# Optimization experiments

Measured on AMD Instinct MI355X. Metric: run time of the kernel, lower is better.

The kernel has to match this reference:

```python
import jax, jax.numpy as jnp
import numpy as np

EPS_LN = 1e-6
NEG_INF = -1e9


def layer_norm(x, gamma, beta, eps=EPS_LN):
    mu = jnp.mean(x, axis=-1, keepdims=True)
    var = jnp.mean(jnp.square(x - mu), axis=-1, keepdims=True)
    return (x - mu) * jax.lax.rsqrt(var + eps) * gamma + beta


def setup_inputs() -> dict:
    key = jax.random.key(0)
    B, S, F, H = 2, 2048, 1024, 16
    D = F // H
    ks = jax.random.split(key, 10)
    s = 1.0 / np.sqrt(F)
    return {
        "x": jax.random.normal(ks[0], (B, S, F), jnp.float32),
        "Wq": jax.random.normal(ks[1], (F, F), jnp.float32) * s,
        "bq": jnp.zeros((F,), jnp.float32),
        "Wk": jax.random.normal(ks[2], (F, F), jnp.float32) * s,
        "bk": jnp.zeros((F,), jnp.float32),
        "Wv": jax.random.normal(ks[3], (F, F), jnp.float32) * s,
        "bv": jnp.zeros((F,), jnp.float32),
        "Wo": jax.random.normal(ks[4], (F, F), jnp.float32) * s,
        "bo": jnp.zeros((F,), jnp.float32),
        "gamma1": jnp.ones((F,), jnp.float32),
        "beta1": jnp.zeros((F,), jnp.float32),
        "gamma2": jnp.ones((F,), jnp.float32),
        "beta2": jnp.zeros((F,), jnp.float32),
        # keras 'uniform' initializer: U(-0.05, 0.05), shape (pos_emb_size=S, depth)
        "pos_emb": jax.random.uniform(ks[5], (S, D), jnp.float32, -0.05, 0.05),
    }


def reference(x, Wq, bq, Wk, bk, Wv, bv, Wo, bo, gamma1, beta1, gamma2, beta2, pos_emb):
    B, S, F = x.shape
    H = 16
    D = F // H
    xn = layer_norm(x, gamma1, beta1)  # pre-LN; also the residual source per original code

    def split_heads(t):
        return t.reshape(B, S, H, D).transpose(0, 2, 1, 3)  # [B,H,S,D]

    q = split_heads(xn @ Wq + bq)
    k = split_heads(xn @ Wk + bk)
    v = split_heads(xn @ Wv + bv)

    # inline position embedding add to K: broadcast [1,1,S,D]
    k = k + pos_emb[None, None, :, :]

    logits = jnp.einsum("bhqd,bhkd->bhqk", q, k) / jnp.sqrt(jnp.float32(D))
    causal = jnp.triu(jnp.ones((S, S), jnp.float32), k=1)  # 1 above diagonal
    logits = logits + causal * NEG_INF
    attn = jax.nn.softmax(logits, axis=-1)  # dropout is identity at inference

    ctx = jnp.einsum("bhqk,bhkd->bhqd", attn, v)
    ctx = ctx.transpose(0, 2, 1, 3).reshape(B, S, F)
    out = ctx @ Wo + bo + xn  # residual with the layernormed input (as in original)
    out = layer_norm(out, gamma2, beta2)
    return out, attn
```

## Files before the change

kernel.cpp:

```cpp
#include <hip/hip_runtime.h>
#include <hip/hip_bf16.h>

#define B_ 2
#define S_ 2048
#define F_ 1024
#define H_ 16
#define D_ 64
#define M_ (B_ * S_)

__global__ void ln_kernel(const float* in, float* out,
                          const float* __restrict__ gamma,
                          const float* __restrict__ beta) {
  int row = blockIdx.x;
  int tid = threadIdx.x;
  const float4* inr = (const float4*)(in + (size_t)row * F_);
  float4 xv = inr[tid];
  float s  = xv.x + xv.y + xv.z + xv.w;
  float s2 = xv.x * xv.x + xv.y * xv.y + xv.z * xv.z + xv.w * xv.w;
#pragma unroll
  for (int off = 32; off > 0; off >>= 1) {
    s  += __shfl_down(s, off, 64);
    s2 += __shfl_down(s2, off, 64);
  }
  __shared__ float red[8];
  int wid = tid >> 6, lane = tid & 63;
  if (lane == 0) { red[wid] = s; red[4 + wid] = s2; }
  __syncthreads();
  if (tid == 0) {
    red[0] = red[0] + red[1] + red[2] + red[3];
    red[4] = red[4] + red[5] + red[6] + red[7];
  }
  __syncthreads();
  float mean = red[0] * (1.0f / F_);
  float var  = red[4] * (1.0f / F_) - mean * mean;
  float rstd = rsqrtf(var + 1e-6f);
  float4 g  = ((const float4*)gamma)[tid];
  float4 be = ((const float4*)beta)[tid];
  float4 o;
  o.x = (xv.x - mean) * rstd * g.x + be.x;
  o.y = (xv.y - mean) * rstd * g.y + be.y;
  o.z = (xv.z - mean) * rstd * g.z + be.z;
  o.w = (xv.w - mean) * rstd * g.w + be.w;
  ((float4*)(out + (size_t)row * F_))[tid] = o;
}

__global__ void gemm_bias(const float* __restrict__ A, const float* __restrict__ W,
                          const float* __restrict__ bias, float* __restrict__ C,
                          const float* R, const float* __restrict__ pos,
                          int mode) {
  const int K = F_, N = F_;
  __shared__ float As[16][132];
  __shared__ float Bs[16][128];
  int tid = threadIdx.x;
  int bm = blockIdx.y * 128, bn = blockIdx.x * 128;
  int tx = tid & 15, ty = tid >> 4;
  float acc[8][8] = {};
  int ar  = tid >> 2;
  int ac  = (tid & 3) << 2;
  int bk  = tid >> 5;
  int bn4 = (tid & 31) << 2;
  const float* Aptr0 = A + (size_t)(bm + ar) * K + ac;
  const float* Aptr1 = Aptr0 + (size_t)64 * K;
  const float* Wptr0 = W + (size_t)bk * N + bn + bn4;
  const float* Wptr1 = Wptr0 + (size_t)8 * N;
  for (int k0 = 0; k0 < K; k0 += 16) {
    float4 a0 = *(const float4*)(Aptr0 + k0);
    float4 a1 = *(const float4*)(Aptr1 + k0);
    float4 b0 = *(const float4*)(Wptr0 + (size_t)k0 * N);
    float4 b1 = *(const float4*)(Wptr1 + (size_t)k0 * N);
    __syncthreads();
    As[ac + 0][ar] = a0.x; As[ac + 1][ar] = a0.y;
    As[ac + 2][ar] = a0.z; As[ac + 3][ar] = a0.w;
    As[ac + 0][ar + 64] = a1.x; As[ac + 1][ar + 64] = a1.y;
    As[ac + 2][ar + 64] = a1.z; As[ac + 3][ar + 64] = a1.w;
    *(float4*)&Bs[bk][bn4]     = b0;
    *(float4*)&Bs[bk + 8][bn4] = b1;
    __syncthreads();
#pragma unroll
    for (int kk = 0; kk < 16; ++kk) {
      float av[8], bv[8];
      *(float4*)(av)     = *(const float4*)&As[kk][ty * 8];
      *(float4*)(av + 4) = *(const float4*)&As[kk][ty * 8 + 4];
      *(float4*)(bv)     = *(const float4*)&Bs[kk][tx * 8];
      *(float4*)(bv + 4) = *(const float4*)&Bs[kk][tx * 8 + 4];
#pragma unroll
      for (int i = 0; i < 8; ++i)
#pragma unroll
        for (int j = 0; j < 8; ++j)
          acc[i][j] += av[i] * bv[j];
    }
  }
#pragma unroll
  for (int i = 0; i < 8; ++i) {
    int m = bm + ty * 8 + i;
#pragma unroll
    for (int j = 0; j < 8; ++j) {
      int n = bn + tx * 8 + j;
      float val = acc[i][j] + bias[n];
      if (mode == 1) val += pos[(size_t)(m & (S_ - 1)) * D_ + (n & (D_ - 1))];
      if (mode == 2) val += R[(size_t)m * N + n];
      C[(size_t)m * N + n] = val;
    }
  }
}

__global__ __launch_bounds__(1024) void attn_kernel(
    const float* q, const float* __restrict__ k, const float* __restrict__ v,
    float* __restrict__ attn, float* ctx, float* __restrict__ rowsum) {
  int bh = blockIdx.y;
  int b = bh >> 4, h = bh & 15;
  int qt = blockIdx.x;
  int tid = threadIdx.x;
  int w = tid >> 6, lane = tid & 63;
  int q_idx = qt * 16 + w;

  __shared__ float K_lds[128][65];
  __shared__ float V_lds[128][64];
  __shared__ float q_lds[16][64];
  __shared__ float p_lds[16][128];

  {
    int r = tid >> 6, c = tid & 63;
    q_lds[r][c] = q[(size_t)(b * S_ + qt * 16 + r) * F_ + h * 64 + c];
  }

  float cacc = 0.0f, ssum = 0.0f;
  int q_max = qt * 16 + 15;
  int nch = (q_max >> 7) + 1;
  const float* Kbase = k + (size_t)b * S_ * F_ + h * 64;
  const float* Vbase = v + (size_t)b * S_ * F_ + h * 64;
  float* arow = attn + ((size_t)bh * S_ + q_idx) * S_;

  for (int c = 0; c < nch; ++c) {
    int base = c << 7;
    __syncthreads();
    for (int idx = tid; idx < 128 * 64; idx += 1024) {
      int r = idx >> 6, cc = idx & 63;
      K_lds[r][cc] = Kbase[(size_t)(base + r) * F_ + cc];
      V_lds[r][cc] = Vbase[(size_t)(base + r) * F_ + cc];
    }
    __syncthreads();
    float acc0 = 0.f, acc1 = 0.f;
#pragma unroll
    for (int d = 0; d < 64; ++d) {
      float qd = q_lds[w][d];
      acc0 += qd * K_lds[lane][d];
      acc1 += qd * K_lds[64 + lane][d];
    }
    int j0 = base + lane, j1 = base + 64 + lane;
    float p0 = 0.f, p1 = 0.f;
    if (j0 <= q_idx) { p0 = __expf(acc0 * 0.125f); arow[j0] = p0; }
    if (j1 <= q_idx) { p1 = __expf(acc1 * 0.125f); arow[j1] = p1; }
    ssum += p0 + p1;
    p_lds[w][lane] = p0;
    p_lds[w][64 + lane] = p1;
    int jmax = q_idx - base + 1;
    if (jmax > 128) jmax = 128;
#pragma unroll 4
    for (int jj = 0; jj < jmax; ++jj)
      cacc += p_lds[w][jj] * V_lds[jj][lane];
  }
  float tot = ssum;
#pragma unroll
  for (int off = 32; off > 0; off >>= 1) tot += __shfl_xor(tot, off, 64);
  float inv = 1.0f / tot;
  ctx[(size_t)(b * S_ + q_idx) * F_ + h * 64 + lane] = cacc * inv;
  if (lane == 0) rowsum[(size_t)bh * S_ + q_idx] = tot;
}

__global__ void rescale_kernel(float* __restrict__ attn,
                               const float* __restrict__ rowsum) {
  int q_idx = blockIdx.x;
  int bh = blockIdx.y;
  float inv = 1.0f / rowsum[(size_t)bh * S_ + q_idx];
  float* arow = attn + ((size_t)bh * S_ + q_idx) * S_;
  int tid = threadIdx.x;
#pragma unroll
  for (int it = 0; it < 2; ++it) {
    int v4 = tid + it * 256;
    int j0 = v4 << 2;
    float4 val;
    if (j0 + 3 <= q_idx) {
      val = ((const float4*)arow)[v4];
      val.x *= inv; val.y *= inv; val.z *= inv; val.w *= inv;
    } else {
      val.x = (j0     <= q_idx) ? arow[j0]     * inv : 0.f;
      val.y = (j0 + 1 <= q_idx) ? arow[j0 + 1] * inv : 0.f;
      val.z = (j0 + 2 <= q_idx) ? arow[j0 + 2] * inv : 0.f;
      val.w = (j0 + 3 <= q_idx) ? arow[j0 + 3] * inv : 0.f;
    }
    ((float4*)arow)[v4] = val;
  }
}

extern "C" void kernel_launch(void* const* d_in, const int* in_sizes, int n_in,
                              void* d_out, int out_size, void* d_ws, size_t ws_size,
                              hipStream_t stream) {
  const float* x      = (const float*)d_in[0];
  const float* Wq     = (const float*)d_in[1];
  const float* bq     = (const float*)d_in[2];
  const float* Wk     = (const float*)d_in[3];
  const float* bk     = (const float*)d_in[4];
  const float* Wv     = (const float*)d_in[5];
  const float* bv     = (const float*)d_in[6];
  const float* Wo     = (const float*)d_in[7];
  const float* bo     = (const float*)d_in[8];
  const float* gamma1 = (const float*)d_in[9];
  const float* beta1  = (const float*)d_in[10];
  const float* gamma2 = (const float*)d_in[11];
  const float* beta2  = (const float*)d_in[12];
  const float* pos    = (const float*)d_in[13];

  float* out  = (float*)d_out;
  float* attn = out + (size_t)M_ * F_;

  float* xn     = (float*)d_ws;
  float* qb     = xn + (size_t)M_ * F_;
  float* kb     = qb + (size_t)M_ * F_;
  float* vb     = kb + (size_t)M_ * F_;
  float* rowsum = vb + (size_t)M_ * F_;
  float* ctx    = qb;

  ln_kernel<<<M_, 256, 0, stream>>>(x, xn, gamma1, beta1);

  dim3 gg(F_ / 128, M_ / 128);
  gemm_bias<<<gg, 256, 0, stream>>>(xn, Wq, bq, qb, nullptr, nullptr, 0);
  gemm_bias<<<gg, 256, 0, stream>>>(xn, Wk, bk, kb, nullptr, pos, 1);
  gemm_bias<<<gg, 256, 0, stream>>>(xn, Wv, bv, vb, nullptr, nullptr, 0);

  attn_kernel<<<dim3(S_ / 16, B_ * H_), 1024, 0, stream>>>(qb, kb, vb, attn, ctx, rowsum);
  rescale_kernel<<<dim3(S_, B_ * H_), 256, 0, stream>>>(attn, rowsum);

  gemm_bias<<<gg, 256, 0, stream>>>(ctx, Wo, bo, out, xn, nullptr, 2);
  ln_kernel<<<M_, 256, 0, stream>>>(out, out, gamma2, beta2);
}
```

Measured before the change: 2.991 ms.

## Use bf16 MFMA GEMMs with transposed weights and swizzled attention LDS

Replaces the fp32 SIMT projection GEMMs with bf16 MFMA 16x16x32 GEMMs. Inputs are loaded straight into LDS with global_load_lds, so the weights are transposed and cast to bf16, and LN1 now writes bf16 output. The attention kernel gets XOR-swizzled K and transposed V LDS layouts with float4 reads, which cuts bank conflicts and scalar LDS traffic. Extra transpose and cast kernels run on every call, and bf16 rounding of the activations and the residual path lowers accuracy.

```diff
diff --git a/kernel.cpp b/kernel.cpp
--- a/kernel.cpp
+++ b/kernel.cpp
@@ -7,6 +7,18 @@
 #define H_ 16
 #define D_ 64
 #define M_ (B_ * S_)
+
+typedef __attribute__((ext_vector_type(8))) short bf16x8;
+typedef __attribute__((ext_vector_type(4))) float f32x4;
+
+__device__ __forceinline__ unsigned short f2bf(float f) {
+  unsigned int u = __float_as_uint(f);
+  u += 0x7fffu + ((u >> 16) & 1u);
+  return (unsigned short)(u >> 16);
+}
+__device__ __forceinline__ float bf2f(unsigned short b) {
+  return __uint_as_float(((unsigned int)b) << 16);
+}
 
 __global__ void ln_kernel(const float* in, float* out,
                           const float* __restrict__ gamma,
@@ -44,64 +56,132 @@
   ((float4*)(out + (size_t)row * F_))[tid] = o;
 }
 
-__global__ void gemm_bias(const float* __restrict__ A, const float* __restrict__ W,
-                          const float* __restrict__ bias, float* __restrict__ C,
-                          const float* R, const float* __restrict__ pos,
-                          int mode) {
-  const int K = F_, N = F_;
-  __shared__ float As[16][132];
-  __shared__ float Bs[16][128];
-  int tid = threadIdx.x;
+__global__ void ln_bf16_kernel(const float* in, unsigned short* outb,
+                               const float* __restrict__ gamma,
+                               const float* __restrict__ beta) {
+  int row = blockIdx.x;
+  int tid = threadIdx.x;
+  const float4* inr = (const float4*)(in + (size_t)row * F_);
+  float4 xv = inr[tid];
+  float s  = xv.x + xv.y + xv.z + xv.w;
+  float s2 = xv.x * xv.x + xv.y * xv.y + xv.z * xv.z + xv.w * xv.w;
+#pragma unroll
+  for (int off = 32; off > 0; off >>= 1) {
+    s  += __shfl_down(s, off, 64);
+    s2 += __shfl_down(s2, off, 64);
+  }
+  __shared__ float red[8];
+  int wid = tid >> 6, lane = tid & 63;
+  if (lane == 0) { red[wid] = s; red[4 + wid] = s2; }
+  __syncthreads();
+  if (tid == 0) {
+    red[0] = red[0] + red[1] + red[2] + red[3];
+    red[4] = red[4] + red[5] + red[6] + red[7];
+  }
+  __syncthreads();
+  float mean = red[0] * (1.0f / F_);
+  float var  = red[4] * (1.0f / F_) - mean * mean;
+  float rstd = rsqrtf(var + 1e-6f);
+  float4 g  = ((const float4*)gamma)[tid];
+  float4 be = ((const float4*)beta)[tid];
+  ushort4 o4;
+  o4.x = f2bf((xv.x - mean) * rstd * g.x + be.x);
+  o4.y = f2bf((xv.y - mean) * rstd * g.y + be.y);
+  o4.z = f2bf((xv.z - mean) * rstd * g.z + be.z);
+  o4.w = f2bf((xv.w - mean) * rstd * g.w + be.w);
+  ((ushort4*)(outb + (size_t)row * F_))[tid] = o4;
+}
+
+__global__ void transpose_cast(const float* __restrict__ W, unsigned short* __restrict__ WT) {
+  __shared__ float t[32][33];
+  int bx = blockIdx.x * 32;
+  int by = blockIdx.y * 32;
+  int tx = threadIdx.x, ty = threadIdx.y;
+#pragma unroll
+  for (int i = 0; i < 32; i += 8)
+    t[ty + i][tx] = W[(size_t)(by + ty + i) * 1024 + bx + tx];
+  __syncthreads();
+#pragma unroll
+  for (int i = 0; i < 32; i += 8)
+    WT[(size_t)(bx + ty + i) * 1024 + by + tx] = f2bf(t[tx][ty + i]);
+}
+
+__global__ void cast_f32_bf16(const float* __restrict__ in, unsigned short* __restrict__ out) {
+  int i = blockIdx.x * 256 + threadIdx.x;
+  float4 v = ((const float4*)in)[i];
+  ushort4 o;
+  o.x = f2bf(v.x); o.y = f2bf(v.y); o.z = f2bf(v.z); o.w = f2bf(v.w);
+  ((ushort4*)out)[i] = o;
+}
+
+template <int MODE>
+__global__ __launch_bounds__(256) void gemm_bf16(
+    const unsigned short* __restrict__ A, const unsigned short* __restrict__ BT,
+    const float* __restrict__ bias, float* __restrict__ C,
+    const unsigned short* __restrict__ resid, const float* __restrict__ pos) {
+  __shared__ unsigned short A_lds[128 * 64];
+  __shared__ unsigned short B_lds[128 * 64];
+  int tid = threadIdx.x;
+  int w = tid >> 6, lane = tid & 63;
   int bm = blockIdx.y * 128, bn = blockIdx.x * 128;
-  int tx = tid & 15, ty = tid >> 4;
-  float acc[8][8] = {};
-  int ar  = tid >> 2;
-  int ac  = (tid & 3) << 2;
-  int bk  = tid >> 5;
-  int bn4 = (tid & 31) << 2;
-  const float* Aptr0 = A + (size_t)(bm + ar) * K + ac;
-  const float* Aptr1 = Aptr0 + (size_t)64 * K;
-  const float* Wptr0 = W + (size_t)bk * N + bn + bn4;
-  const float* Wptr1 = Wptr0 + (size_t)8 * N;
-  for (int k0 = 0; k0 < K; k0 += 16) {
-    float4 a0 = *(const float4*)(Aptr0 + k0);
-    float4 a1 = *(const float4*)(Aptr1 + k0);
-    float4 b0 = *(const float4*)(Wptr0 + (size_t)k0 * N);
-    float4 b1 = *(const float4*)(Wptr1 + (size_t)k0 * N);
+  int wm = w >> 1, wn = w & 1;
+
+  f32x4 zero = {0.f, 0.f, 0.f, 0.f};
+  f32x4 acc[4][4];
+#pragma unroll
+  for (int i = 0; i < 4; ++i)
+#pragma unroll
+    for (int j = 0; j < 4; ++j) acc[i][j] = zero;
+
+  for (int k0 = 0; k0 < 1024; k0 += 64) {
+#pragma unroll
+    for (int i = 0; i < 4; ++i) {
+      int li = (w * 4 + i) * 64 + lane;
+      int row = li >> 3, g = li & 7;
+      const unsigned short* ga = A  + (size_t)(bm + row) * 1024 + k0 + g * 8;
+      const unsigned short* gb = BT + (size_t)(bn + row) * 1024 + k0 + g * 8;
+      __builtin_amdgcn_global_load_lds(
+          (const __attribute__((address_space(1))) unsigned int*)ga,
+          (__attribute__((address_space(3))) unsigned int*)&A_lds[(w * 4 + i) * 512],
+          16, 0, 0);
+      __builtin_amdgcn_global_load_lds(
+          (const __attribute__((address_space(1))) unsigned int*)gb,
+          (__attribute__((address_space(3))) unsigned int*)&B_lds[(w * 4 + i) * 512],
+          16, 0, 0);
+    }
     __syncthreads();
-    As[ac + 0][ar] = a0.x; As[ac + 1][ar] = a0.y;
-    As[ac + 2][ar] = a0.z; As[ac + 3][ar] = a0.w;
-    As[ac + 0][ar + 64] = a1.x; As[ac + 1][ar + 64] = a1.y;
-    As[ac + 2][ar + 64] = a1.z; As[ac + 3][ar + 64] = a1.w;
-    *(float4*)&Bs[bk][bn4]     = b0;
-    *(float4*)&Bs[bk + 8][bn4] = b1;
+#pragma unroll
+    for (int ks = 0; ks < 64; ks += 32) {
+      bf16x8 a[4], b[4];
+#pragma unroll
+      for (int mf = 0; mf < 4; ++mf)
+        a[mf] = *(const bf16x8*)&A_lds[(wm * 64 + mf * 16 + (lane & 15)) * 64 + ks + (lane >> 4) * 8];
+#pragma unroll
+      for (int nf = 0; nf < 4; ++nf)
+        b[nf] = *(const bf16x8*)&B_lds[(wn * 64 + nf * 16 + (lane & 15)) * 64 + ks + (lane >> 4) * 8];
+#pragma unroll
+      for (int mf = 0; mf < 4; ++mf)
+#pragma unroll
+        for (int nf = 0; nf < 4; ++nf)
+          acc[mf][nf] = __builtin_amdgcn_mfma_f32_16x16x32_bf16(a[mf], b[nf], acc[mf][nf], 0, 0, 0);
+    }
     __syncthreads();
-#pragma unroll
-    for (int kk = 0; kk < 16; ++kk) {
-      float av[8], bv[8];
-      *(float4*)(av)     = *(const float4*)&As[kk][ty * 8];
-      *(float4*)(av + 4) = *(const float4*)&As[kk][ty * 8 + 4];
-      *(float4*)(bv)     = *(const float4*)&Bs[kk][tx * 8];
-      *(float4*)(bv + 4) = *(const float4*)&Bs[kk][tx * 8 + 4];
-#pragma unroll
-      for (int i = 0; i < 8; ++i)
-#pragma unroll
-        for (int j = 0; j < 8; ++j)
-          acc[i][j] += av[i] * bv[j];
-    }
-  }
-#pragma unroll
-  for (int i = 0; i < 8; ++i) {
-    int m = bm + ty * 8 + i;
-#pragma unroll
-    for (int j = 0; j < 8; ++j) {
-      int n = bn + tx * 8 + j;
-      float val = acc[i][j] + bias[n];
-      if (mode == 1) val += pos[(size_t)(m & (S_ - 1)) * D_ + (n & (D_ - 1))];
-      if (mode == 2) val += R[(size_t)m * N + n];
-      C[(size_t)m * N + n] = val;
-    }
-  }
+  }
+
+  int lr = (lane >> 4) * 4, lc = lane & 15;
+#pragma unroll
+  for (int mf = 0; mf < 4; ++mf)
+#pragma unroll
+    for (int nf = 0; nf < 4; ++nf)
+#pragma unroll
+      for (int r = 0; r < 4; ++r) {
+        int m = bm + wm * 64 + mf * 16 + lr + r;
+        int n = bn + wn * 64 + nf * 16 + lc;
+        float val = acc[mf][nf][r] + bias[n];
+        if (MODE == 1) val += pos[(size_t)(m & (S_ - 1)) * D_ + (n & (D_ - 1))];
+        if (MODE == 2) val += bf2f(resid[(size_t)m * 1024 + n]);
+        C[(size_t)m * 1024 + n] = val;
+      }
 }
 
 __global__ __launch_bounds__(1024) void attn_kernel(
@@ -114,8 +194,8 @@
   int w = tid >> 6, lane = tid & 63;
   int q_idx = qt * 16 + w;
 
-  __shared__ float K_lds[128][65];
-  __shared__ float V_lds[128][64];
+  __shared__ float K_lds[128 * 64];
+  __shared__ float Vt_lds[64 * 128];
   __shared__ float q_lds[16][64];
   __shared__ float p_lds[16][128];
 
@@ -130,22 +210,31 @@
   const float* Kbase = k + (size_t)b * S_ * F_ + h * 64;
   const float* Vbase = v + (size_t)b * S_ * F_ + h * 64;
   float* arow = attn + ((size_t)bh * S_ + q_idx) * S_;
+  int sw = lane & 7;
 
   for (int c = 0; c < nch; ++c) {
     int base = c << 7;
     __syncthreads();
-    for (int idx = tid; idx < 128 * 64; idx += 1024) {
-      int r = idx >> 6, cc = idx & 63;
-      K_lds[r][cc] = Kbase[(size_t)(base + r) * F_ + cc];
-      V_lds[r][cc] = Vbase[(size_t)(base + r) * F_ + cc];
+    for (int idx = tid; idx < 2048; idx += 1024) {
+      int r = idx >> 4, c4 = idx & 15;
+      float4 gk = *(const float4*)&Kbase[(size_t)(base + r) * F_ + (c4 << 2)];
+      *(float4*)&K_lds[r * 64 + ((c4 ^ (r & 7)) << 2)] = gk;
+      float4 gv = *(const float4*)&Vbase[(size_t)(base + r) * F_ + (c4 << 2)];
+      int c0 = c4 << 2, g = r >> 2, ro = r & 3;
+      Vt_lds[(c0 + 0) * 128 + ((g ^ ((c0 + 0) & 7)) << 2) + ro] = gv.x;
+      Vt_lds[(c0 + 1) * 128 + ((g ^ ((c0 + 1) & 7)) << 2) + ro] = gv.y;
+      Vt_lds[(c0 + 2) * 128 + ((g ^ ((c0 + 2) & 7)) << 2) + ro] = gv.z;
+      Vt_lds[(c0 + 3) * 128 + ((g ^ ((c0 + 3) & 7)) << 2) + ro] = gv.w;
     }
     __syncthreads();
     float acc0 = 0.f, acc1 = 0.f;
 #pragma unroll
-    for (int d = 0; d < 64; ++d) {
-      float qd = q_lds[w][d];
-      acc0 += qd * K_lds[lane][d];
-      acc1 += qd * K_lds[64 + lane][d];
+    for (int d4 = 0; d4 < 16; ++d4) {
+      float4 q4 = *(const float4*)&q_lds[w][d4 << 2];
+      float4 ka = *(const float4*)&K_lds[lane * 64 + ((d4 ^ sw) << 2)];
+      float4 kb = *(const float4*)&K_lds[(64 + lane) * 64 + ((d4 ^ sw) << 2)];
+      acc0 += q4.x * ka.x; acc0 += q4.y * ka.y; acc0 += q4.z * ka.z; acc0 += q4.w * ka.w;
+      acc1 += q4.x * kb.x; acc1 += q4.y * kb.y; acc1 += q4.z * kb.z; acc1 += q4.w * kb.w;
     }
     int j0 = base + lane, j1 = base + 64 + lane;
     float p0 = 0.f, p1 = 0.f;
@@ -156,9 +245,13 @@
     p_lds[w][64 + lane] = p1;
     int jmax = q_idx - base + 1;
     if (jmax > 128) jmax = 128;
+    int nj4 = (jmax + 3) >> 2;
 #pragma unroll 4
-    for (int jj = 0; jj < jmax; ++jj)
-      cacc += p_lds[w][jj] * V_lds[jj][lane];
+    for (int jj4 = 0; jj4 < nj4; ++jj4) {
+      float4 p4 = *(const float4*)&p_lds[w][jj4 << 2];
+      float4 v4 = *(const float4*)&Vt_lds[lane * 128 + ((jj4 ^ sw) << 2)];
+      cacc += p4.x * v4.x; cacc += p4.y * v4.y; cacc += p4.z * v4.z; cacc += p4.w * v4.w;
+    }
   }
   float tot = ssum;
 #pragma unroll
@@ -214,23 +307,35 @@
   float* out  = (float*)d_out;
   float* attn = out + (size_t)M_ * F_;
 
-  float* xn     = (float*)d_ws;
-  float* qb     = xn + (size_t)M_ * F_;
-  float* kb     = qb + (size_t)M_ * F_;
-  float* vb     = kb + (size_t)M_ * F_;
-  float* rowsum = vb + (size_t)M_ * F_;
-  float* ctx    = qb;
-
-  ln_kernel<<<M_, 256, 0, stream>>>(x, xn, gamma1, beta1);
+  unsigned char* ws = (unsigned char*)d_ws;
+  float* qb             = (float*)(ws + (size_t)(0u  << 20));
+  float* kb             = (float*)(ws + (size_t)(16u << 20));
+  float* vb             = (float*)(ws + (size_t)(32u << 20));
+  unsigned short* ctxb  = (unsigned short*)(ws + (size_t)(32u << 20));
+  unsigned short* xnb   = (unsigned short*)(ws + (size_t)(48u << 20));
+  unsigned short* WqT   = (unsigned short*)(ws + (size_t)(56u << 20));
+  unsigned short* WkT   = (unsigned short*)(ws + (size_t)(58u << 20));
+  unsigned short* WvT   = (unsigned short*)(ws + (size_t)(60u << 20));
+  unsigned short* WoT   = (unsigned short*)(ws + (size_t)(62u << 20));
+  float* rowsum         = (float*)(ws + (size_t)(64u << 20));
+
+  dim3 tb(32, 8), tg(32, 32);
+  transpose_cast<<<tg, tb, 0, stream>>>(Wq, WqT);
+  transpose_cast<<<tg, tb, 0, stream>>>(Wk, WkT);
+  transpose_cast<<<tg, tb, 0, stream>>>(Wv, WvT);
+  transpose_cast<<<tg, tb, 0, stream>>>(Wo, WoT);
+
+  ln_bf16_kernel<<<M_, 256, 0, stream>>>(x, xnb, gamma1, beta1);
 
   dim3 gg(F_ / 128, M_ / 128);
-  gemm_bias<<<gg, 256, 0, stream>>>(xn, Wq, bq, qb, nullptr, nullptr, 0);
-  gemm_bias<<<gg, 256, 0, stream>>>(xn, Wk, bk, kb, nullptr, pos, 1);
-  gemm_bias<<<gg, 256, 0, stream>>>(xn, Wv, bv, vb, nullptr, nullptr, 0);
-
-  attn_kernel<<<dim3(S_ / 16, B_ * H_), 1024, 0, stream>>>(qb, kb, vb, attn, ctx, rowsum);
+  gemm_bf16<0><<<gg, 256, 0, stream>>>(xnb, WqT, bq, qb, nullptr, nullptr);
+  gemm_bf16<1><<<gg, 256, 0, stream>>>(xnb, WkT, bk, kb, nullptr, pos);
+  gemm_bf16<0><<<gg, 256, 0, stream>>>(xnb, WvT, bv, vb, nullptr, nullptr);
+
+  attn_kernel<<<dim3(S_ / 16, B_ * H_), 1024, 0, stream>>>(qb, kb, vb, attn, qb, rowsum);
   rescale_kernel<<<dim3(S_, B_ * H_), 256, 0, stream>>>(attn, rowsum);
 
-  gemm_bias<<<gg, 256, 0, stream>>>(ctx, Wo, bo, out, xn, nullptr, 2);
+  cast_f32_bf16<<<(M_ * F_ / 4) / 256, 256, 0, stream>>>(qb, ctxb);
+  gemm_bf16<2><<<gg, 256, 0, stream>>>(ctxb, WoT, bo, out, xnb, nullptr);
   ln_kernel<<<M_, 256, 0, stream>>>(out, out, gamma2, beta2);
 }
```

After: 3.002 ms. About the same (+0.4%).
